# Kernel optimization log

Measured on AMD Instinct MI355X. Metric: run time of the kernel, lower is better.

Reference implementation:

```python
import jax, jax.numpy as jnp
import numpy as np

DECAY = 0.99
EPSILON = 1e-05
N_TOKENS = 32768
EMBED_DIM = 256
NUM_EMB = 4096


def setup_inputs() -> dict:
    key = jax.random.key(0)
    k1, k2, k3 = jax.random.split(key, 3)
    return {
        "inputs": jax.random.normal(k1, (N_TOKENS, EMBED_DIM), dtype=jnp.float32),
        "codebook": jax.random.normal(k2, (NUM_EMB, EMBED_DIM), dtype=jnp.float32),
        "ema_w": jax.random.normal(k3, (NUM_EMB, EMBED_DIM), dtype=jnp.float32),
        "ema_cluster_size": jnp.zeros((NUM_EMB,), dtype=jnp.float32),
    }


def reference(inputs, codebook, ema_w, ema_cluster_size):
    K, D = codebook.shape
    flat = inputs.reshape(-1, D)  # [N, D]
    distances = (
        jnp.sum(flat * flat, axis=1, keepdims=True)
        + jnp.sum(codebook * codebook, axis=1)
        - 2.0 * flat @ codebook.T
    )
    encoding_indices = jnp.argmin(distances, axis=1)  # [N]
    encodings = jax.nn.one_hot(encoding_indices, K, dtype=flat.dtype)  # [N, K]
    quantized = codebook[encoding_indices].reshape(inputs.shape)  # [N, D]

    # EMA update (training branch). dw = encodings.T @ flat expressed as a
    # segment sum to avoid a second [N,K]-sized contraction pass.
    dw = jax.ops.segment_sum(flat, encoding_indices, num_segments=K)  # [K, D]
    counts = jax.ops.segment_sum(
        jnp.ones((flat.shape[0],), dtype=flat.dtype), encoding_indices, num_segments=K
    )  # [K]
    new_ema_w = ema_w * DECAY + (1.0 - DECAY) * dw
    cs = ema_cluster_size * DECAY + (1.0 - DECAY) * counts
    n = jnp.sum(cs)
    cs = (cs + EPSILON) / (n + K * EPSILON) * n  # laplace smoothing
    new_codebook = new_ema_w / cs[:, None]
    return quantized, encodings, new_codebook, new_ema_w, cs
```

## Files before the change

kernel.cpp:

```cpp
#include <hip/hip_runtime.h>
#include <hip/hip_bf16.h>

#define NTOK 32768
#define KEMB 4096
#define DDIM 256
#define DECAYF 0.99f
#define EPSF 1e-5f
#define KSPLIT 256
#define FLAG_THETA 0.09f
#define PRUNE_MARGIN 0.25f

#define B_AHAT  0ull
#define B_BHAT  16777216ull
#define B_PART  18874368ull
#define B_CE    52428800ull
#define B_CNTI  52445184ull
#define B_CSP   52461568ull
#define B_OFFS  52477952ull
#define B_NPTR  52494336ull
#define B_TIDX  52494400ull
#define B_FLIST 52625472ull
#define B_SLOT  52756544ull
#define B_TLIST 52887616ull
#define B_DW    53018688ull

#define OFF_Q  0ull
#define OFF_E  8388608ull
#define OFF_CB 142606336ull
#define OFF_W  143654912ull
#define OFF_CS 144703488ull

typedef __attribute__((ext_vector_type(8))) _Float16 f16x8;
typedef __attribute__((ext_vector_type(4))) float f32x4;

__global__ __launch_bounds__(256) void cast16_kernel(const float* __restrict__ src,
                                                     _Float16* __restrict__ dst) {
    size_t gid = (size_t)blockIdx.x * 256 + threadIdx.x;
    const float* sp = src + gid * 8;
    f16x8 v;
    #pragma unroll
    for (int t = 0; t < 8; ++t) v[t] = (_Float16)sp[t];
    *(f16x8*)(dst + gid * 8) = v;
}

__global__ __launch_bounds__(256) void ce_kernel(const float* __restrict__ cb,
                                                 float* __restrict__ ce) {
    int k = blockIdx.x * 4 + (threadIdx.x >> 6);
    int lane = threadIdx.x & 63;
    float4 v = *(const float4*)(cb + (size_t)k * DDIM + lane * 4);
    float s = v.x * v.x + v.y * v.y + v.z * v.z + v.w * v.w;
    #pragma unroll
    for (int o = 32; o > 0; o >>= 1) s += __shfl_down(s, o);
    if (lane == 0) ce[k] = s;
}

__global__ __launch_bounds__(256) void gemm_argmin_kernel(
        const _Float16* __restrict__ Ahat,
        const _Float16* __restrict__ Bhat,
        const float* __restrict__ ceg,
        float4* __restrict__ part) {
    __shared__ _Float16 As[128 * 64];
    __shared__ _Float16 Bs[128 * 64];
    const int tid  = threadIdx.x;
    const int lane = tid & 63;
    const int wave = tid >> 6;
    const int wm = wave >> 1, wn = wave & 1;
    const int nb = blockIdx.x, mb = blockIdx.y;
    const int col = lane & 15, q = lane >> 4;
    const int cswz = q ^ (col & 7);

    const int srow = tid >> 3;
    const int sswz = (tid & 7) ^ (srow & 7);
    const _Float16* ag = Ahat + (size_t)(mb * 128 + srow) * KSPLIT + sswz * 8;
    const _Float16* bg = Bhat + (size_t)(nb * 128 + srow) * KSPLIT + sswz * 8;

    f32x4 zero = {0.f, 0.f, 0.f, 0.f};
    f32x4 acc[4][4];
    #pragma unroll
    for (int i = 0; i < 4; ++i)
        #pragma unroll
        for (int j = 0; j < 4; ++j) acc[i][j] = zero;

    for (int kt = 0; kt < KSPLIT / 64; ++kt) {
        __syncthreads();
        #pragma unroll
        for (int n = 0; n < 4; ++n) {
            __builtin_amdgcn_global_load_lds(
                (const __attribute__((address_space(1))) void*)(ag + (size_t)n * 32 * KSPLIT + kt * 64),
                (__attribute__((address_space(3))) void*)(As + n * 2048 + tid * 8), 16, 0, 0);
            __builtin_amdgcn_global_load_lds(
                (const __attribute__((address_space(1))) void*)(bg + (size_t)n * 32 * KSPLIT + kt * 64),
                (__attribute__((address_space(3))) void*)(Bs + n * 2048 + tid * 8), 16, 0, 0);
        }
        __syncthreads();

        const f16x8* Av = (const f16x8*)As;
        const f16x8* Bv = (const f16x8*)Bs;
        #pragma unroll
        for (int ks = 0; ks < 2; ++ks) {
            f16x8 a[4], b[4];
            #pragma unroll
            for (int i = 0; i < 4; ++i)
                a[i] = Av[(wm * 64 + i * 16 + col) * 8 + (cswz ^ (ks * 4))];
            #pragma unroll
            for (int j = 0; j < 4; ++j)
                b[j] = Bv[(wn * 64 + j * 16 + col) * 8 + (cswz ^ (ks * 4))];
            #pragma unroll
            for (int i = 0; i < 4; ++i)
                #pragma unroll
                for (int j = 0; j < 4; ++j)
                    acc[i][j] = __builtin_amdgcn_mfma_f32_16x16x32_f16(a[i], b[j], acc[i][j], 0, 0, 0);
        }
    }

    float ce_j[4];
    #pragma unroll
    for (int j = 0; j < 4; ++j) ce_j[j] = ceg[nb * 128 + wn * 64 + j * 16 + col];

    #pragma unroll
    for (int i = 0; i < 4; ++i) {
        #pragma unroll
        for (int r = 0; r < 4; ++r) {
            float b1 = 3.4e38f, b2 = 3.4e38f;
            int i1 = 0x7fffffff;
            #pragma unroll
            for (int j = 0; j < 4; ++j) {
                float s = ce_j[j] - 2.0f * acc[i][j][r];
                int n = nb * 128 + wn * 64 + j * 16 + col;
                if (s < b1) { b2 = b1; b1 = s; i1 = n; }
                else if (s < b2) { b2 = s; }
            }
            #pragma unroll
            for (int m = 1; m < 16; m <<= 1) {
                float ob1 = __shfl_xor(b1, m, 16);
                float ob2 = __shfl_xor(b2, m, 16);
                int   oi  = __shfl_xor(i1, m, 16);
                bool take = (ob1 < b1) || (ob1 == b1 && oi < i1);
                float nb2 = take ? fminf(b1, ob2) : fminf(b2, ob1);
                if (take) { b1 = ob1; i1 = oi; }
                b2 = nb2;
            }
            if (col == i * 4 + r) {
                int mrow = mb * 128 + wm * 64 + i * 16 + q * 4 + r;
                float4 p;
                p.x = b1; p.y = b2; p.z = __int_as_float(i1); p.w = 0.0f;
                part[(size_t)mrow * 64 + nb * 2 + wn] = p;
            }
        }
    }
}

__global__ __launch_bounds__(256) void argmin_reduce_kernel(
        const float4* __restrict__ part,
        int* __restrict__ tokIdx,
        int* __restrict__ flist,
        int* __restrict__ flagCount) {
    int row = blockIdx.x * 4 + (threadIdx.x >> 6);
    int lane = threadIdx.x & 63;
    float4 p = part[(size_t)row * 64 + lane];
    float b1 = p.x, b2 = p.y;
    int i1 = __float_as_int(p.z);
    #pragma unroll
    for (int m = 1; m < 64; m <<= 1) {
        float ob1 = __shfl_xor(b1, m);
        float ob2 = __shfl_xor(b2, m);
        int   oi  = __shfl_xor(i1, m);
        bool take = (ob1 < b1) || (ob1 == b1 && oi < i1);
        float nb2 = take ? fminf(b1, ob2) : fminf(b2, ob1);
        if (take) { b1 = ob1; i1 = oi; }
        b2 = nb2;
    }
    if (lane == 0) {
        tokIdx[row] = i1;
        if (b2 - b1 < FLAG_THETA) {
            int slot = atomicAdd(flagCount, 1);
            flist[slot] = row;
        }
    }
}

__global__ __launch_bounds__(256) void refine_kernel(const float* __restrict__ xg,
                                                     const float* __restrict__ cb,
                                                     const float4* __restrict__ part,
                                                     int* __restrict__ tokIdx,
                                                     const int* __restrict__ flagList,
                                                     const int* __restrict__ flagCount) {
    int nf = *flagCount;
    int lane = threadIdx.x & 63;
    int wid = (blockIdx.x * 256 + threadIdx.x) >> 6;
    int nw = (gridDim.x * 256) >> 6;
    for (int f = wid; f < nf; f += nw) {
        int tok = flagList[f];
        float cb1 = part[(size_t)tok * 64 + lane].x;
        float b1 = cb1;
        #pragma unroll
        for (int m = 1; m < 64; m <<= 1) b1 = fminf(b1, __shfl_xor(b1, m));
        unsigned long long mask = __ballot(cb1 <= b1 + PRUNE_MARGIN);
        double best = 1e300;
        int bi = 0x7fffffff;
        const float* xr = xg + (size_t)tok * DDIM;
        while (mask) {
            int c = __ffsll(mask) - 1;
            mask &= mask - 1;
            int k = c * 64 + lane;
            const float* e = cb + (size_t)k * DDIM;
            double s = 0.0;
            for (int d4 = 0; d4 < DDIM / 4; ++d4) {
                float4 e4 = *(const float4*)(e + d4 * 4);
                float4 x4 = *(const float4*)(xr + d4 * 4);
                double e0 = (double)e4.x, e1 = (double)e4.y;
                double e2 = (double)e4.z, e3 = (double)e4.w;
                s += e0 * (e0 - 2.0 * (double)x4.x) + e1 * (e1 - 2.0 * (double)x4.y)
                   + e2 * (e2 - 2.0 * (double)x4.z) + e3 * (e3 - 2.0 * (double)x4.w);
            }
            if (s < best || (s == best && k < bi)) { best = s; bi = k; }
        }
        #pragma unroll
        for (int m = 1; m < 64; m <<= 1) {
            double ob = __shfl_xor(best, m);
            int   oi  = __shfl_xor(bi, m);
            if (ob < best || (ob == best && oi < bi)) { best = ob; bi = oi; }
        }
        if (lane == 0) tokIdx[tok] = bi;
    }
}

__global__ __launch_bounds__(256) void tokslot_kernel(const int* __restrict__ tokIdx,
                                                      int* __restrict__ countsI,
                                                      int* __restrict__ slotOf) {
    int t = blockIdx.x * 256 + threadIdx.x;
    int k = tokIdx[t];
    slotOf[t] = atomicAdd(countsI + k, 1);
}

__global__ __launch_bounds__(256) void scan_kernel(const int* __restrict__ countsI,
                                                   int* __restrict__ offs) {
    __shared__ int part[256];
    __shared__ int pref[257];
    int tid = threadIdx.x;
    int local[16];
    int s = 0;
    #pragma unroll
    for (int i = 0; i < 16; ++i) { local[i] = countsI[tid * 16 + i]; s += local[i]; }
    part[tid] = s;
    __syncthreads();
    if (tid == 0) {
        pref[0] = 0;
        for (int i = 0; i < 256; ++i) pref[i + 1] = pref[i] + part[i];
    }
    __syncthreads();
    int run = pref[tid];
    #pragma unroll
    for (int i = 0; i < 16; ++i) { offs[tid * 16 + i] = run; run += local[i]; }
}

__global__ __launch_bounds__(256) void filllist_kernel(const int* __restrict__ tokIdx,
                                                       const int* __restrict__ offs,
                                                       const int* __restrict__ slotOf,
                                                       int* __restrict__ tlist) {
    int t = blockIdx.x * 256 + threadIdx.x;
    int k = tokIdx[t];
    tlist[offs[k] + slotOf[t]] = t;
}

__global__ __launch_bounds__(256) void cs_kernel(const float* __restrict__ ema_cs,
                                                 const int* __restrict__ countsI,
                                                 float* __restrict__ cs_pre,
                                                 float* __restrict__ nptr) {
    int k = blockIdx.x * 256 + threadIdx.x;
    float c = ema_cs[k] * DECAYF + (1.0f - DECAYF) * (float)countsI[k];
    cs_pre[k] = c;
    float s = c;
    #pragma unroll
    for (int o = 32; o > 0; o >>= 1) s += __shfl_down(s, o);
    __shared__ float red[4];
    int lane = threadIdx.x & 63, w = threadIdx.x >> 6;
    if (lane == 0) red[w] = s;
    __syncthreads();
    if (threadIdx.x == 0) atomicAdd(nptr, red[0] + red[1] + red[2] + red[3]);
}

__global__ __launch_bounds__(256) void scatter_kernel(const float* __restrict__ cb,
                                                      const int* __restrict__ tokIdx,
                                                      float* __restrict__ quant,
                                                      float* __restrict__ enc) {
    int tok = blockIdx.x;
    int tid = threadIdx.x;
    int k = tokIdx[tok];
    float4* er = (float4*)(enc + (size_t)tok * KEMB);
    int kf4 = k >> 2, kc = k & 3;
    #pragma unroll
    for (int v = 0; v < 4; ++v) {
        int f4 = v * 256 + tid;
        float4 val = {0.f, 0.f, 0.f, 0.f};
        if (f4 == kf4) ((float*)&val)[kc] = 1.0f;
        er[f4] = val;
    }
    if (tid < 64) {
        float4 e = *(const float4*)(cb + (size_t)k * DDIM + tid * 4);
        *(float4*)(quant + (size_t)tok * DDIM + tid * 4) = e;
    }
}

#define SEG_CHUNK 32
__global__ __launch_bounds__(256) void segdw_kernel(const float* __restrict__ xg,
                                                    const int* __restrict__ tlist,
                                                    const int* __restrict__ tokIdx,
                                                    float* __restrict__ dw) {
    int tid = threadIdx.x;
    int s0 = blockIdx.x * SEG_CHUNK;
    float acc = 0.0f;
    int curk = -1;
    for (int s = s0; s < s0 + SEG_CHUNK; ++s) {
        int t = tlist[s];
        int k = tokIdx[t];
        if (k != curk) {
            if (curk >= 0) atomicAdd(dw + (size_t)curk * DDIM + tid, acc);
            acc = 0.0f;
            curk = k;
        }
        acc += xg[(size_t)t * DDIM + tid];
    }
    if (curk >= 0) atomicAdd(dw + (size_t)curk * DDIM + tid, acc);
}

__global__ __launch_bounds__(256) void epi_kernel(const float* __restrict__ ema_w,
                                                  const float* __restrict__ dw,
                                                  const float* __restrict__ cs_pre,
                                                  const float* __restrict__ nptr,
                                                  float* __restrict__ new_cb,
                                                  float* __restrict__ new_w,
                                                  float* __restrict__ cs_out) {
    int gid = blockIdx.x * 256 + threadIdx.x;
    int k = gid >> 8, d = gid & 255;
    float n = *nptr;
    float csp = cs_pre[k];
    float cs = (csp + EPSF) / (n + (float)KEMB * EPSF) * n;
    float w = ema_w[gid] * DECAYF + (1.0f - DECAYF) * dw[gid];
    new_w[gid] = w;
    new_cb[gid] = w / cs;
    if (d == 0) cs_out[k] = cs;
}

extern "C" void kernel_launch(void* const* d_in, const int* in_sizes, int n_in,
                              void* d_out, int out_size, void* d_ws, size_t ws_size,
                              hipStream_t stream) {
    const float* xg     = (const float*)d_in[0];
    const float* cbg    = (const float*)d_in[1];
    const float* ema_w  = (const float*)d_in[2];
    const float* ema_cs = (const float*)d_in[3];

    float* out = (float*)d_out;
    unsigned char* wsb = (unsigned char*)d_ws;

    float* quant  = out + OFF_Q;
    float* enc    = out + OFF_E;
    float* new_cb = out + OFF_CB;
    float* new_w  = out + OFF_W;
    float* cs_out = out + OFF_CS;

    _Float16* Ahat = (_Float16*)(wsb + B_AHAT);
    _Float16* Bhat = (_Float16*)(wsb + B_BHAT);
    float4* part   = (float4*)(wsb + B_PART);
    float* ce      = (float*)(wsb + B_CE);
    int*   countsI = (int*)(wsb + B_CNTI);
    float* cs_pre  = (float*)(wsb + B_CSP);
    int*   offs    = (int*)(wsb + B_OFFS);
    float* nptr    = (float*)(wsb + B_NPTR);
    int*   flagCnt = (int*)(wsb + B_NPTR + 4);
    int*   tokIdx  = (int*)(wsb + B_TIDX);
    int*   flist   = (int*)(wsb + B_FLIST);
    int*   slotOf  = (int*)(wsb + B_SLOT);
    int*   tlist   = (int*)(wsb + B_TLIST);
    float* dw      = (float*)(wsb + B_DW);

    hipMemsetAsync(countsI, 0, KEMB * sizeof(int), stream);
    hipMemsetAsync(nptr, 0, 8, stream);
    hipMemsetAsync(dw, 0, (size_t)KEMB * DDIM * sizeof(float), stream);

    cast16_kernel<<<(NTOK * DDIM / 8) / 256, 256, 0, stream>>>(xg, Ahat);
    cast16_kernel<<<(KEMB * DDIM / 8) / 256, 256, 0, stream>>>(cbg, Bhat);
    ce_kernel<<<KEMB / 4, 256, 0, stream>>>(cbg, ce);
    gemm_argmin_kernel<<<dim3(KEMB / 128, NTOK / 128), 256, 0, stream>>>(Ahat, Bhat, ce, part);
    argmin_reduce_kernel<<<NTOK / 4, 256, 0, stream>>>(part, tokIdx, flist, flagCnt);
    refine_kernel<<<256, 256, 0, stream>>>(xg, cbg, part, tokIdx, flist, flagCnt);
    tokslot_kernel<<<NTOK / 256, 256, 0, stream>>>(tokIdx, countsI, slotOf);
    cs_kernel<<<KEMB / 256, 256, 0, stream>>>(ema_cs, countsI, cs_pre, nptr);
    scan_kernel<<<1, 256, 0, stream>>>(countsI, offs);
    filllist_kernel<<<NTOK / 256, 256, 0, stream>>>(tokIdx, offs, slotOf, tlist);
    scatter_kernel<<<NTOK, 256, 0, stream>>>(cbg, tokIdx, quant, enc);
    segdw_kernel<<<NTOK / SEG_CHUNK, 256, 0, stream>>>(xg, tlist, tokIdx, dw);
    epi_kernel<<<(KEMB * DDIM) / 256, 256, 0, stream>>>(ema_w, dw, cs_pre, nptr,
                                                        new_cb, new_w, cs_out);
}
```

Before: 855.2 us.

## Fuse codebook cast with norms, merge scatter/slot and scan/cs kernels, swizzle GEMM blocks

Merges the codebook fp16 cast into the norm kernel and folds the token-slot atomics, quantized gather and one-hot write into a single finalize kernel. The cluster-size EMA and its total now come from the single-block scan kernel, which removes one launch and an atomic. The one-hot matrix is zero-filled with a memset instead of per-element kernel stores. The GEMM also remaps block indices, so blocks launched together share A/B tiles for better L2 reuse. The cost is serial float summation in one thread and a separate 512MB memset plus scattered single-element writes.

```diff
diff --git a/kernel.cpp b/kernel.cpp
--- a/kernel.cpp
+++ b/kernel.cpp
@@ -31,6 +31,7 @@
 #define OFF_CS 144703488ull
 
 typedef __attribute__((ext_vector_type(8))) _Float16 f16x8;
+typedef __attribute__((ext_vector_type(4))) _Float16 f16x4;
 typedef __attribute__((ext_vector_type(4))) float f32x4;
 
 __global__ __launch_bounds__(256) void cast16_kernel(const float* __restrict__ src,
@@ -43,11 +44,16 @@
     *(f16x8*)(dst + gid * 8) = v;
 }
 
-__global__ __launch_bounds__(256) void ce_kernel(const float* __restrict__ cb,
-                                                 float* __restrict__ ce) {
+__global__ __launch_bounds__(256) void castcb_ce_kernel(const float* __restrict__ cb,
+                                                        _Float16* __restrict__ Bhat,
+                                                        float* __restrict__ ce) {
     int k = blockIdx.x * 4 + (threadIdx.x >> 6);
     int lane = threadIdx.x & 63;
     float4 v = *(const float4*)(cb + (size_t)k * DDIM + lane * 4);
+    f16x4 h;
+    h[0] = (_Float16)v.x; h[1] = (_Float16)v.y;
+    h[2] = (_Float16)v.z; h[3] = (_Float16)v.w;
+    *(f16x4*)(Bhat + (size_t)k * DDIM + lane * 4) = h;
     float s = v.x * v.x + v.y * v.y + v.z * v.z + v.w * v.w;
     #pragma unroll
     for (int o = 32; o > 0; o >>= 1) s += __shfl_down(s, o);
@@ -65,7 +71,11 @@
     const int lane = tid & 63;
     const int wave = tid >> 6;
     const int wm = wave >> 1, wn = wave & 1;
-    const int nb = blockIdx.x, mb = blockIdx.y;
+
+    int lin = blockIdx.y * 32 + blockIdx.x;
+    lin = (lin & 7) * 1024 + (lin >> 3);
+    const int nb = lin & 31, mb = lin >> 5;
+
     const int col = lane & 15, q = lane >> 4;
     const int cswz = q ^ (col & 7);
 
@@ -225,28 +235,55 @@
     }
 }
 
-__global__ __launch_bounds__(256) void tokslot_kernel(const int* __restrict__ tokIdx,
-                                                      int* __restrict__ countsI,
-                                                      int* __restrict__ slotOf) {
-    int t = blockIdx.x * 256 + threadIdx.x;
+__global__ __launch_bounds__(256) void finalize_kernel(const float* __restrict__ cb,
+                                                       const int* __restrict__ tokIdx,
+                                                       int* __restrict__ countsI,
+                                                       int* __restrict__ slotOf,
+                                                       float* __restrict__ quant,
+                                                       float* __restrict__ enc) {
+    int t = blockIdx.x * 4 + (threadIdx.x >> 6);
+    int lane = threadIdx.x & 63;
     int k = tokIdx[t];
-    slotOf[t] = atomicAdd(countsI + k, 1);
-}
-
-__global__ __launch_bounds__(256) void scan_kernel(const int* __restrict__ countsI,
-                                                   int* __restrict__ offs) {
+    if (lane == 0) {
+        slotOf[t] = atomicAdd(countsI + k, 1);
+        enc[(size_t)t * KEMB + k] = 1.0f;
+    }
+    float4 e = *(const float4*)(cb + (size_t)k * DDIM + lane * 4);
+    *(float4*)(quant + (size_t)t * DDIM + lane * 4) = e;
+}
+
+__global__ __launch_bounds__(256) void scan_cs_kernel(const int* __restrict__ countsI,
+                                                      const float* __restrict__ ema_cs,
+                                                      int* __restrict__ offs,
+                                                      float* __restrict__ cs_pre,
+                                                      float* __restrict__ nptr) {
     __shared__ int part[256];
+    __shared__ float npart[256];
     __shared__ int pref[257];
     int tid = threadIdx.x;
     int local[16];
     int s = 0;
-    #pragma unroll
-    for (int i = 0; i < 16; ++i) { local[i] = countsI[tid * 16 + i]; s += local[i]; }
+    float ns = 0.0f;
+    #pragma unroll
+    for (int i = 0; i < 16; ++i) {
+        int c = countsI[tid * 16 + i];
+        local[i] = c;
+        s += c;
+        float csp = ema_cs[tid * 16 + i] * DECAYF + (1.0f - DECAYF) * (float)c;
+        cs_pre[tid * 16 + i] = csp;
+        ns += csp;
+    }
     part[tid] = s;
+    npart[tid] = ns;
     __syncthreads();
     if (tid == 0) {
         pref[0] = 0;
-        for (int i = 0; i < 256; ++i) pref[i + 1] = pref[i] + part[i];
+        float nn = 0.0f;
+        for (int i = 0; i < 256; ++i) {
+            pref[i + 1] = pref[i] + part[i];
+            nn += npart[i];
+        }
+        nptr[0] = nn;
     }
     __syncthreads();
     int run = pref[tid];
@@ -261,45 +298,6 @@
     int t = blockIdx.x * 256 + threadIdx.x;
     int k = tokIdx[t];
     tlist[offs[k] + slotOf[t]] = t;
-}
-
-__global__ __launch_bounds__(256) void cs_kernel(const float* __restrict__ ema_cs,
-                                                 const int* __restrict__ countsI,
-                                                 float* __restrict__ cs_pre,
-                                                 float* __restrict__ nptr) {
-    int k = blockIdx.x * 256 + threadIdx.x;
-    float c = ema_cs[k] * DECAYF + (1.0f - DECAYF) * (float)countsI[k];
-    cs_pre[k] = c;
-    float s = c;
-    #pragma unroll
-    for (int o = 32; o > 0; o >>= 1) s += __shfl_down(s, o);
-    __shared__ float red[4];
-    int lane = threadIdx.x & 63, w = threadIdx.x >> 6;
-    if (lane == 0) red[w] = s;
-    __syncthreads();
-    if (threadIdx.x == 0) atomicAdd(nptr, red[0] + red[1] + red[2] + red[3]);
-}
-
-__global__ __launch_bounds__(256) void scatter_kernel(const float* __restrict__ cb,
-                                                      const int* __restrict__ tokIdx,
-                                                      float* __restrict__ quant,
-                                                      float* __restrict__ enc) {
-    int tok = blockIdx.x;
-    int tid = threadIdx.x;
-    int k = tokIdx[tok];
-    float4* er = (float4*)(enc + (size_t)tok * KEMB);
-    int kf4 = k >> 2, kc = k & 3;
-    #pragma unroll
-    for (int v = 0; v < 4; ++v) {
-        int f4 = v * 256 + tid;
-        float4 val = {0.f, 0.f, 0.f, 0.f};
-        if (f4 == kf4) ((float*)&val)[kc] = 1.0f;
-        er[f4] = val;
-    }
-    if (tid < 64) {
-        float4 e = *(const float4*)(cb + (size_t)k * DDIM + tid * 4);
-        *(float4*)(quant + (size_t)tok * DDIM + tid * 4) = e;
-    }
 }
 
 #define SEG_CHUNK 32
@@ -374,21 +372,19 @@
     int*   tlist   = (int*)(wsb + B_TLIST);
     float* dw      = (float*)(wsb + B_DW);
 
+    hipMemsetAsync(enc, 0, (size_t)NTOK * KEMB * sizeof(float), stream);
     hipMemsetAsync(countsI, 0, KEMB * sizeof(int), stream);
     hipMemsetAsync(nptr, 0, 8, stream);
     hipMemsetAsync(dw, 0, (size_t)KEMB * DDIM * sizeof(float), stream);
 
     cast16_kernel<<<(NTOK * DDIM / 8) / 256, 256, 0, stream>>>(xg, Ahat);
-    cast16_kernel<<<(KEMB * DDIM / 8) / 256, 256, 0, stream>>>(cbg, Bhat);
-    ce_kernel<<<KEMB / 4, 256, 0, stream>>>(cbg, ce);
+    castcb_ce_kernel<<<KEMB / 4, 256, 0, stream>>>(cbg, Bhat, ce);
     gemm_argmin_kernel<<<dim3(KEMB / 128, NTOK / 128), 256, 0, stream>>>(Ahat, Bhat, ce, part);
     argmin_reduce_kernel<<<NTOK / 4, 256, 0, stream>>>(part, tokIdx, flist, flagCnt);
     refine_kernel<<<256, 256, 0, stream>>>(xg, cbg, part, tokIdx, flist, flagCnt);
-    tokslot_kernel<<<NTOK / 256, 256, 0, stream>>>(tokIdx, countsI, slotOf);
-    cs_kernel<<<KEMB / 256, 256, 0, stream>>>(ema_cs, countsI, cs_pre, nptr);
-    scan_kernel<<<1, 256, 0, stream>>>(countsI, offs);
+    finalize_kernel<<<NTOK / 4, 256, 0, stream>>>(cbg, tokIdx, countsI, slotOf, quant, enc);
+    scan_cs_kernel<<<1, 256, 0, stream>>>(countsI, ema_cs, offs, cs_pre, nptr);
     filllist_kernel<<<NTOK / 256, 256, 0, stream>>>(tokIdx, offs, slotOf, tlist);
-    scatter_kernel<<<NTOK, 256, 0, stream>>>(cbg, tokIdx, quant, enc);
     segdw_kernel<<<NTOK / SEG_CHUNK, 256, 0, stream>>>(xg, tlist, tokIdx, dw);
     epi_kernel<<<(KEMB * DDIM) / 256, 256, 0, stream>>>(ema_w, dw, cs_pre, nptr,
                                                         new_cb, new_w, cs_out);
```

Measured after the change: 835.0 us. -2.4%, faster.
